# Kernel optimization log

Hardware: AMD Instinct MI355X
Metric: run time of the kernel (lower is better)

Reference implementation:

```python
import jax, jax.numpy as jnp
import numpy as np
from jax import lax

DIM = 192
HEADS = 6
WIDTH = 256
HEIGHT = 128
BATCH = 2


def _conv1x1(x, w):
    # x: [b,c,h,w], w: [o,c] (1x1 conv, no bias)
    return jnp.einsum('bchw,oc->bohw', x, w)


def setup_inputs() -> dict:
    key = jax.random.key(0)
    ks = jax.random.split(key, 7)
    c = DIM
    std = c ** -0.5
    x = jax.random.normal(ks[0], (BATCH, c, HEIGHT, WIDTH), dtype=jnp.float32)
    rpb_table = 0.02 * jax.random.normal(ks[1], (2 * WIDTH - 1, HEADS), dtype=jnp.float32)
    w_qkv = std * jax.random.normal(ks[2], (3 * c, c), dtype=jnp.float32)
    w_depth = (1.0 / 3.0) * jax.random.normal(ks[3], (3 * c, 1, 3, 3), dtype=jnp.float32)
    w_pre = std * jax.random.normal(ks[4], (c, c), dtype=jnp.float32)
    w_out = std * jax.random.normal(ks[5], (c, c), dtype=jnp.float32)
    w_gate = std * jax.random.normal(ks[6], (c, c), dtype=jnp.float32)
    return {"x": x, "rpb_table": rpb_table, "w_qkv": w_qkv, "w_depth": w_depth,
            "w_pre": w_pre, "w_out": w_out, "w_gate": w_gate, "num_heads": HEADS}


def reference(x, rpb_table, w_qkv, w_depth, w_pre, w_out, w_gate, num_heads):
    b, c, h, w = x.shape
    hd = c // num_heads
    scale = hd ** -0.5

    x_gate = jax.nn.silu(_conv1x1(x, w_gate))

    t = _conv1x1(x, w_qkv)  # [b, 3c, h, w]
    qkv = lax.conv_general_dilated(
        t, w_depth, window_strides=(1, 1), padding='SAME',
        feature_group_count=3 * c,
        dimension_numbers=('NCHW', 'OIHW', 'NCHW'))
    q, k, v = jnp.split(qkv, 3, axis=1)

    def _rows(z):
        # 'b (head c) h w -> b h head w c'
        return z.reshape(b, num_heads, hd, h, w).transpose(0, 3, 1, 4, 2)

    q = _rows(q) * scale
    k = _rows(k)
    v = _rows(v)

    attn = jnp.einsum('bhnic,bhnjc->bhnij', q, k)  # [b, h, heads, w, w]

    # relative position bias: index[i, j] = i - j + (w - 1)
    idx = jnp.arange(w)[:, None] - jnp.arange(w)[None, :] + (w - 1)
    bias = rpb_table[idx].transpose(2, 0, 1)  # [heads, w, w]
    attn = jax.nn.softmax(attn + bias[None, None], axis=-1)

    out = jnp.einsum('bhnij,bhnjc->bhnic', attn, v)
    # 'b h head w c -> b (head c) h w'
    out = out.transpose(0, 2, 4, 1, 3).reshape(b, c, h, w)

    out = _conv1x1(out, w_pre) * x_gate
    return _conv1x1(out, w_out)
```

## Files before the change

kernel.cpp:

```cpp
#include <hip/hip_runtime.h>
#include <hip/hip_bf16.h>
#include <math.h>

#define BATCH 2
#define C 192
#define H 128
#define W 256
#define HEADS 6
#define HD 32
#define HW (H * W)
#define C3 (3 * C)
#define NPX (BATCH * HW)

typedef unsigned short ushort_t;
using bf16x8 = __attribute__((ext_vector_type(8))) short;
using f32x4  = __attribute__((ext_vector_type(4))) float;

static __device__ __forceinline__ float bfbits2f(ushort_t u) {
    return __uint_as_float(((unsigned)u) << 16);
}
static __device__ __forceinline__ ushort_t f2bfbits(float f) {
    __hip_bfloat16 h = __float2bfloat16(f);
    return *reinterpret_cast<ushort_t*>(&h);
}

__global__ __launch_bounds__(256) void prep_w_kernel(
    const float* __restrict__ wq, const float* __restrict__ wg,
    const float* __restrict__ wp, const float* __restrict__ wo,
    ushort_t* __restrict__ dst)
{
    const int i = blockIdx.x * 256 + threadIdx.x;
    const float* src; int off, base;
    if (i < 27648)      { src = wq; off = i;         base = 0; }
    else if (i < 36864) { src = wg; off = i - 27648; base = 110592; }
    else if (i < 46080) { src = wp; off = i - 36864; base = 147456; }
    else                { src = wo; off = i - 46080; base = 184320; }
    float4 v = ((const float4*)src)[off];
    if (i < 9216) {
        const float sc = 0.25503488f;
        v.x *= sc; v.y *= sc; v.z *= sc; v.w *= sc;
    }
    ushort4 o;
    o.x = f2bfbits(v.x); o.y = f2bfbits(v.y);
    o.z = f2bfbits(v.z); o.w = f2bfbits(v.w);
    *(ushort4*)(dst + base + off * 4) = o;
}

__global__ __launch_bounds__(256) void transpose_x_kernel(
    const float* __restrict__ x, ushort_t* __restrict__ xt)
{
    __shared__ uint Xs[64 * 97];
    const int p0 = blockIdx.x * 64;
    const int b  = p0 >> 15, hw0 = p0 & (HW - 1);
    const int t  = threadIdx.x;

    {
        const int px = t & 63, g = t >> 6;
        const float* xb = x + (size_t)b * C * HW + hw0 + px;
#pragma unroll
        for (int i = 0; i < 24; ++i) {
            const int cp = g + i * 4;
            const float v0 = xb[(size_t)(2 * cp) * HW];
            const float v1 = xb[(size_t)(2 * cp + 1) * HW];
            Xs[px * 97 + cp] = (uint)f2bfbits(v0) | ((uint)f2bfbits(v1) << 16);
        }
    }
    __syncthreads();
    {
        const int px = t >> 2, grp = t & 3;
        uint* dst = (uint*)(xt + (size_t)(p0 + px) * C) + grp * 24;
        const uint* s = &Xs[px * 97 + grp * 24];
#pragma unroll
        for (int i = 0; i < 6; ++i) {
            uint4 u;
            u.x = s[i * 4 + 0]; u.y = s[i * 4 + 1];
            u.z = s[i * 4 + 2]; u.w = s[i * 4 + 3];
            *(uint4*)(dst + i * 4) = u;
        }
    }
}

template <int MODE, int OUTKIND, int MT>
__global__ __launch_bounds__(256, 2) void conv_mfma_kernel(
    const ushort_t* __restrict__ in_t, const ushort_t* __restrict__ w_bf,
    void* __restrict__ outp, ushort_t* __restrict__ gate, int ostride)
{
    const int lin = blockIdx.x;
    const int xcd = lin & 7;
    const int jj  = lin >> 3;
    const int pin = jj / MT;
    const int m   = jj - pin * MT;
    const int m0  = m * 64;
    const int p0  = (xcd * 32 + pin) * 256;

    const int t  = threadIdx.x;
    const int wv = t >> 6, lane = t & 63, quad = lane >> 4, l16 = lane & 15;

    __shared__ ushort_t smem[18432];
    ushort_t* As = smem;

    const ushort_t* bp = in_t + (size_t)(p0 + wv * 64 + l16) * C + quad * 8;
    bf16x8 bF[6][4];
#pragma unroll
    for (int ks = 0; ks < 6; ++ks)
#pragma unroll
        for (int ct = 0; ct < 4; ++ct)
            bF[ks][ct] = *(const bf16x8*)(bp + (size_t)(ct * 16) * C + ks * 32);

    {
        const int row = t >> 2, cg = (t & 3) * 48;
        const ushort_t* src = w_bf + (size_t)(m0 + row) * C + cg;
        ushort_t* dst = &As[row * 200 + cg];
#pragma unroll
        for (int i = 0; i < 6; ++i)
            *(bf16x8*)(dst + i * 8) = *(const bf16x8*)(src + i * 8);
    }
    __syncthreads();

    f32x4 acc[4][4];
#pragma unroll
    for (int rt = 0; rt < 4; ++rt)
#pragma unroll
        for (int ct = 0; ct < 4; ++ct) acc[rt][ct] = f32x4{0.f, 0.f, 0.f, 0.f};

#pragma unroll
    for (int ks = 0; ks < 6; ++ks) {
        bf16x8 aF[4];
#pragma unroll
        for (int rt = 0; rt < 4; ++rt)
            aF[rt] = *(const bf16x8*)&As[(rt * 16 + l16) * 200 + quad * 8 + ks * 32];
#pragma unroll
        for (int rt = 0; rt < 4; ++rt)
#pragma unroll
            for (int ct = 0; ct < 4; ++ct)
                acc[rt][ct] = __builtin_amdgcn_mfma_f32_16x16x32_bf16(
                    aF[rt], bF[ks][ct], acc[rt][ct], 0, 0, 0);
    }

    const bool isg = (MODE == 3) && (m >= 9);
    if (MODE == 1 || isg) {
#pragma unroll
        for (int rt = 0; rt < 4; ++rt)
#pragma unroll
            for (int ct = 0; ct < 4; ++ct) {
                f32x4 v = acc[rt][ct];
#pragma unroll
                for (int r = 0; r < 4; ++r)
                    v[r] = v[r] / (1.f + __expf(-v[r]));
                acc[rt][ct] = v;
            }
    }

    if constexpr (OUTKIND == 0) {
        __syncthreads();
        ushort_t* Ls = smem;
#pragma unroll
        for (int rt = 0; rt < 4; ++rt)
#pragma unroll
            for (int ct = 0; ct < 4; ++ct) {
                const f32x4 v = acc[rt][ct];
                ushort4 o;
                o.x = f2bfbits(v[0]); o.y = f2bfbits(v[1]);
                o.z = f2bfbits(v[2]); o.w = f2bfbits(v[3]);
                *(ushort4*)&Ls[(wv * 64 + ct * 16 + l16) * 72 +
                               rt * 16 + quad * 4] = o;
            }
        __syncthreads();

        ushort_t* ob; int osr, chb;
        if constexpr (MODE == 3) {
            ob  = isg ? gate : (ushort_t*)outp;
            osr = isg ? C : C3;
            chb = isg ? m0 - C3 : m0;
        } else {
            ob = (ushort_t*)outp; osr = ostride; chb = m0;
        }
        const int pxl = t >> 3, c8 = (t & 7) * 8;
#pragma unroll
        for (int r = 0; r < 8; ++r) {
            const int px = r * 32 + pxl;
            const bf16x8 v = *(const bf16x8*)&Ls[px * 72 + c8];
            *(bf16x8*)(ob + (size_t)(p0 + px) * osr + chb + c8) = v;
        }
    } else {
        const int bb = p0 >> 15;
        const int hwb = (p0 & (HW - 1)) + wv * 64;
        float* ob = (float*)outp + ((size_t)bb * C + m0) * HW + hwb;
#pragma unroll
        for (int rt = 0; rt < 4; ++rt)
#pragma unroll
            for (int ct = 0; ct < 4; ++ct) {
                const f32x4 v = acc[rt][ct];
#pragma unroll
                for (int r = 0; r < 4; ++r)
                    ob[(size_t)(rt * 16 + quad * 4 + r) * HW + ct * 16 + l16] = v[r];
            }
    }
}

__global__ __launch_bounds__(256) void dwconv3x3_px_kernel(
    const ushort_t* __restrict__ tin, const float* __restrict__ wd,
    ushort_t* __restrict__ out)
{
    __shared__ float wloc[576];
    __shared__ ushort_t Ld[128 * 72];
    const int bx = blockIdx.x;
    const int px_blk = (bx & 7) * 64 + (63 - (bx >> 3));
    const int cb  = blockIdx.y;
    const int tid = threadIdx.x;
    if (tid < 144)
        *(float4*)&wloc[tid * 4] = *(const float4*)(wd + cb * 576 + tid * 4);
    __syncthreads();

    const int chloc = (tid & 7) * 8;
    const int pxl0 = (tid >> 3) * 4;
    const int px = px_blk * 128 + pxl0;
    const int x0 = px & (W - 1);
    const int y  = (px >> 8) & (H - 1);

    const ushort_t* tb = tin + (size_t)px * C3 + cb * 64 + chloc;

    float acc[4][8];
#pragma unroll
    for (int i = 0; i < 4; ++i)
#pragma unroll
        for (int k = 0; k < 8; ++k) acc[i][k] = 0.f;

#pragma unroll
    for (int dy = -1; dy <= 1; ++dy) {
        const int yy = y + dy;
        if (yy < 0 || yy >= H) continue;
        const ushort_t* rp = tb + (ptrdiff_t)dy * W * C3;

        float f[6][8];
#pragma unroll
        for (int d = 0; d < 6; ++d) {
            const int xx = x0 + d - 1;
            if (xx < 0 || xx >= W) {
#pragma unroll
                for (int k = 0; k < 8; ++k) f[d][k] = 0.f;
            } else {
                const bf16x8 v = *(const bf16x8*)(rp + (ptrdiff_t)(d - 1) * C3);
#pragma unroll
                for (int k = 0; k < 8; ++k) f[d][k] = bfbits2f((ushort_t)v[k]);
            }
        }
#pragma unroll
        for (int k = 0; k < 8; ++k) {
            const float* wk = &wloc[(chloc + k) * 9 + (dy + 1) * 3];
            const float w0 = wk[0], w1 = wk[1], w2 = wk[2];
#pragma unroll
            for (int i = 0; i < 4; ++i)
                acc[i][k] += f[i][k] * w0 + f[i + 1][k] * w1 + f[i + 2][k] * w2;
        }
    }

#pragma unroll
    for (int i = 0; i < 4; ++i) {
        bf16x8 o;
#pragma unroll
        for (int k = 0; k < 8; ++k) o[k] = (short)f2bfbits(acc[i][k]);
        *(bf16x8*)&Ld[(pxl0 + i) * 72 + chloc] = o;
    }
    __syncthreads();

    const int pxl = tid >> 3, c8 = (tid & 7) * 8;
#pragma unroll
    for (int r = 0; r < 4; ++r) {
        const int p = r * 32 + pxl;
        const bf16x8 v = *(const bf16x8*)&Ld[p * 72 + c8];
        *(bf16x8*)(out + (size_t)(px_blk * 128 + p) * C3 + cb * 64 + c8) = v;
    }
}

__global__ __launch_bounds__(256, 4) void attention_mfma_kernel(
    const ushort_t* __restrict__ qkv, const float* __restrict__ rpb,
    ushort_t* __restrict__ att)
{
    const int lin  = blockIdx.x;
    const int xcd  = lin & 7;
    const int j    = lin >> 3;
    const int b    = xcd >> 2;
    const int y    = (xcd & 3) * 32 + (j & 31);
    const int head = j >> 5;
    const int t    = threadIdx.x;
    const int wv   = t >> 6;
    const int lane = t & 63;
    const int quad = lane >> 4;
    const int l16  = lane & 15;

    __shared__ __align__(16) char smem[39424];
    ushort_t* Vt = (ushort_t*)smem;
    ushort_t* Pb = (ushort_t*)(smem + 16896);
    ushort_t* rb = (ushort_t*)(smem + 37376);
    float*    Ol = (float*)smem;

    const size_t rowbase = ((size_t)b * HW + (size_t)y * W) * C3;
    const ushort_t* qbase = qkv + rowbase + head * HD + quad * 8;
    const ushort_t* kbase = qbase + C;

    {
        const ushort_t* rowp = qkv + rowbase + (size_t)t * C3 + head * HD;
        bf16x8 vfr[4];
#pragma unroll
        for (int g = 0; g < 4; ++g)
            vfr[g] = *(const bf16x8*)(rowp + 2 * C + g * 8);
#pragma unroll
        for (int g = 0; g < 4; ++g)
#pragma unroll
            for (int k = 0; k < 8; ++k)
                Vt[(g * 8 + k) * 264 + t] = (ushort_t)vfr[g][k];
    }
    {
        const float LOG2E = 1.4426950408889634f;
#pragma unroll
        for (int s2 = 0; s2 < 2; ++s2)
#pragma unroll
            for (int pp = 0; pp < 2; ++pp) {
                const int k = pp * 256 + t;
                const int src = k + s2;
                rb[s2 * 512 + k] =
                    f2bfbits(src <= 510 ? rpb[src * HEADS + head] * LOG2E : 0.f);
            }
    }

    bf16x8 aQ[4];
#pragma unroll
    for (int rt = 0; rt < 4; ++rt)
        aQ[rt] = *(const bf16x8*)(qbase + (size_t)(wv * 64 + rt * 16 + l16) * C3);
    bf16x8 bK = *(const bf16x8*)(kbase + (size_t)l16 * C3);

    __syncthreads();

    ushort_t* PbW = Pb + wv * 2560;
    float lsum[4] = {0.f, 0.f, 0.f, 0.f};
    f32x4 o_acc[4][2];
#pragma unroll
    for (int rt = 0; rt < 4; ++rt)
#pragma unroll
        for (int ct = 0; ct < 2; ++ct)
            o_acc[rt][ct] = f32x4{0.f, 0.f, 0.f, 0.f};

    const int ibase = wv * 64 + l16 + 255 - quad * 4;

    for (int c2 = 0; c2 < 8; ++c2) {
#pragma unroll
        for (int half = 0; half < 2; ++half) {
            const int n  = c2 * 2 + half;
            const int nn = (n < 15) ? n + 1 : 15;
            const bf16x8 bKn =
                *(const bf16x8*)(kbase + (size_t)(nn * 16 + l16) * C3);
#pragma unroll
            for (int rt = 0; rt < 4; ++rt) {
                const int a  = ibase + rt * 16 - n * 16 - 3;
                const int s2 = a & 1;
                const uint* tp = (const uint*)(rb + s2 * 512 + (a - s2));
                const uint u0 = tp[0], u1 = tp[1];
                f32x4 s;
                s[0] = __uint_as_float(u1 & 0xffff0000u);
                s[1] = __uint_as_float(u1 << 16);
                s[2] = __uint_as_float(u0 & 0xffff0000u);
                s[3] = __uint_as_float(u0 << 16);
                s = __builtin_amdgcn_mfma_f32_16x16x32_bf16(bK, aQ[rt], s, 0, 0, 0);
                const float p0 = __builtin_amdgcn_exp2f(s[0]);
                const float p1 = __builtin_amdgcn_exp2f(s[1]);
                const float p2 = __builtin_amdgcn_exp2f(s[2]);
                const float p3 = __builtin_amdgcn_exp2f(s[3]);
                lsum[rt] += (p0 + p1) + (p2 + p3);
                uint2 dd;
                dd.x = (uint)f2bfbits(p0) | ((uint)f2bfbits(p1) << 16);
                dd.y = (uint)f2bfbits(p2) | ((uint)f2bfbits(p3) << 16);
                *(uint2*)&PbW[(rt * 16 + l16) * 40 + half * 16 + quad * 4] = dd;
            }
            bK = bKn;
        }
#pragma unroll
        for (int rt = 0; rt < 4; ++rt) {
            const bf16x8 aP = *(const bf16x8*)&PbW[(rt * 16 + l16) * 40 + quad * 8];
#pragma unroll
            for (int ct = 0; ct < 2; ++ct) {
                const bf16x8 bV = *(const bf16x8*)
                    &Vt[(ct * 16 + l16) * 264 + c2 * 32 + quad * 8];
                o_acc[rt][ct] = __builtin_amdgcn_mfma_f32_16x16x32_bf16(
                    aP, bV, o_acc[rt][ct], 0, 0, 0);
            }
        }
    }

    float linv[4];
#pragma unroll
    for (int rt = 0; rt < 4; ++rt) {
        float v = lsum[rt];
        v += __shfl_xor(v, 16);
        v += __shfl_xor(v, 32);
        linv[rt] = 1.f / v;
    }

    __syncthreads();
#pragma unroll
    for (int rt = 0; rt < 4; ++rt) {
        const int i = wv * 64 + rt * 16 + quad * 4;
        float sc[4];
#pragma unroll
        for (int reg = 0; reg < 4; ++reg)
            sc[reg] = __shfl(linv[rt], quad * 4 + reg);
#pragma unroll
        for (int ct = 0; ct < 2; ++ct) {
            const int c = ct * 16 + l16;
#pragma unroll
            for (int reg = 0; reg < 4; ++reg)
                Ol[c * 257 + i + reg] = o_acc[rt][ct][reg] * sc[reg];
        }
    }
    __syncthreads();

    const size_t orow = (size_t)b * HW + (size_t)y * W;
    const int pxl = t >> 2, part = t & 3;
#pragma unroll
    for (int r = 0; r < 4; ++r) {
        const int px = r * 64 + pxl;
        bf16x8 o;
#pragma unroll
        for (int k = 0; k < 8; ++k)
            o[k] = (short)f2bfbits(Ol[(part * 8 + k) * 257 + px]);
        *(bf16x8*)(att + (orow + px) * C + head * HD + part * 8) = o;
    }
}

__global__ __launch_bounds__(256, 3) void conv2_fused_kernel(
    const ushort_t* __restrict__ att_t, const ushort_t* __restrict__ gatep,
    const ushort_t* __restrict__ wpre, const ushort_t* __restrict__ wout,
    float* __restrict__ outp)
{
    const int lin = blockIdx.x;
    const int xcd = lin & 7;
    const int pin = lin >> 3;
    const int p0  = (xcd * 64 + pin) * 128;

    const int t  = threadIdx.x;
    const int wv = t >> 6, lane = t & 63, quad = lane >> 4, l16 = lane & 15;

    __shared__ ushort_t Zs[4][32 * 200];
    ushort_t* Zw = Zs[wv];
    const int pxw = p0 + wv * 32;

#pragma unroll
    for (int ms = 0; ms < 3; ++ms) {
        f32x4 acc[4][2];
#pragma unroll
        for (int rt = 0; rt < 4; ++rt)
#pragma unroll
            for (int ct = 0; ct < 2; ++ct) acc[rt][ct] = f32x4{0.f,0.f,0.f,0.f};

        const ushort_t* ap = wpre + (size_t)(ms * 64 + l16) * C + quad * 8;
        const ushort_t* bp = att_t + (size_t)(pxw + l16) * C + quad * 8;
#pragma unroll
        for (int ks = 0; ks < 6; ++ks) {
            bf16x8 aF[4];
#pragma unroll
            for (int rt = 0; rt < 4; ++rt)
                aF[rt] = *(const bf16x8*)(ap + (size_t)(rt * 16) * C + ks * 32);
            const bf16x8 b0 = *(const bf16x8*)(bp + ks * 32);
            const bf16x8 b1 = *(const bf16x8*)(bp + (size_t)16 * C + ks * 32);
#pragma unroll
            for (int rt = 0; rt < 4; ++rt) {
                acc[rt][0] = __builtin_amdgcn_mfma_f32_16x16x32_bf16(
                    aF[rt], b0, acc[rt][0], 0, 0, 0);
                acc[rt][1] = __builtin_amdgcn_mfma_f32_16x16x32_bf16(
                    aF[rt], b1, acc[rt][1], 0, 0, 0);
            }
        }
#pragma unroll
        for (int rt = 0; rt < 4; ++rt)
#pragma unroll
            for (int ct = 0; ct < 2; ++ct) {
                const int px = pxw + ct * 16 + l16;
                const int ch = ms * 64 + rt * 16 + quad * 4;
                const ushort4 g = *(const ushort4*)(gatep + (size_t)px * C + ch);
                f32x4 v = acc[rt][ct];
                v[0] *= bfbits2f(g.x); v[1] *= bfbits2f(g.y);
                v[2] *= bfbits2f(g.z); v[3] *= bfbits2f(g.w);
                ushort4 o;
                o.x = f2bfbits(v[0]); o.y = f2bfbits(v[1]);
                o.z = f2bfbits(v[2]); o.w = f2bfbits(v[3]);
                *(ushort4*)&Zw[(ct * 16 + l16) * 200 + ch] = o;
            }
    }

    const int bb  = p0 >> 15;
    const int hwb = (p0 & (HW - 1)) + wv * 32;
#pragma unroll
    for (int ms = 0; ms < 3; ++ms) {
        f32x4 acc[4][2];
#pragma unroll
        for (int rt = 0; rt < 4; ++rt)
#pragma unroll
            for (int ct = 0; ct < 2; ++ct) acc[rt][ct] = f32x4{0.f,0.f,0.f,0.f};

        const ushort_t* ap = wout + (size_t)(ms * 64 + l16) * C + quad * 8;
#pragma unroll
        for (int ks = 0; ks < 6; ++ks) {
            bf16x8 aF[4];
#pragma unroll
            for (int rt = 0; rt < 4; ++rt)
                aF[rt] = *(const bf16x8*)(ap + (size_t)(rt * 16) * C + ks * 32);
            const bf16x8 b0 = *(const bf16x8*)&Zw[l16 * 200 + quad * 8 + ks * 32];
            const bf16x8 b1 = *(const bf16x8*)&Zw[(16 + l16) * 200 + quad * 8 + ks * 32];
#pragma unroll
            for (int rt = 0; rt < 4; ++rt) {
                acc[rt][0] = __builtin_amdgcn_mfma_f32_16x16x32_bf16(
                    aF[rt], b0, acc[rt][0], 0, 0, 0);
                acc[rt][1] = __builtin_amdgcn_mfma_f32_16x16x32_bf16(
                    aF[rt], b1, acc[rt][1], 0, 0, 0);
            }
        }
        float* ob = outp + ((size_t)bb * C + ms * 64) * HW + hwb;
#pragma unroll
        for (int rt = 0; rt < 4; ++rt)
#pragma unroll
            for (int ct = 0; ct < 2; ++ct) {
                const f32x4 v = acc[rt][ct];
#pragma unroll
                for (int r = 0; r < 4; ++r)
                    __builtin_nontemporal_store(v[r],
                        &ob[(size_t)(rt * 16 + quad * 4 + r) * HW + ct * 16 + l16]);
            }
    }
}

extern "C" void kernel_launch(void* const* d_in, const int* in_sizes, int n_in,
                              void* d_out, int out_size, void* d_ws, size_t ws_size,
                              hipStream_t stream)
{
    const float* x       = (const float*)d_in[0];
    const float* rpb     = (const float*)d_in[1];
    const float* w_qkv   = (const float*)d_in[2];
    const float* w_depth = (const float*)d_in[3];
    const float* w_pre   = (const float*)d_in[4];
    const float* w_out   = (const float*)d_in[5];
    const float* w_gate  = (const float*)d_in[6];
    float* out = (float*)d_out;

    char* wsb = (char*)d_ws;
    ushort_t* wbf      = (ushort_t*)wsb;
    ushort_t* w_pre_b  = wbf + 147456;
    ushort_t* w_out_b  = wbf + 184320;
    ushort_t* gate_t   = (ushort_t*)(wsb + 524288u);
    ushort_t* buf_t    = (ushort_t*)(wsb + 25690112u);
    ushort_t* att_t    = (ushort_t*)(wsb + 25690112u);
    ushort_t* buf_qkv  = (ushort_t*)(wsb + 101187584u);
    ushort_t* x_t      = (ushort_t*)(wsb + 101187584u);

    dim3 blk(256);

    prep_w_kernel<<<dim3(216), blk, 0, stream>>>(w_qkv, w_gate, w_pre, w_out, wbf);
    transpose_x_kernel<<<dim3(NPX / 64), blk, 0, stream>>>(x, x_t);
    conv_mfma_kernel<3, 0, 12><<<dim3(3072), blk, 0, stream>>>(
        x_t, wbf, buf_t, gate_t, C3);
    dwconv3x3_px_kernel<<<dim3(NPX / 128, 9), blk, 0, stream>>>(
        buf_t, w_depth, buf_qkv);
    attention_mfma_kernel<<<dim3(H * HEADS * BATCH), blk, 0, stream>>>(
        buf_qkv, rpb, att_t);
    conv2_fused_kernel<<<dim3(NPX / 128), blk, 0, stream>>>(
        att_t, gate_t, w_pre_b, w_out_b, out);
}
```

Baseline: 285.6 us.

## Batch global loads ahead of use with asm barriers across all kernels

Adds an empty inline-asm KEEP macro that pins loaded values in registers, so each kernel issues all of its global loads before any consumer arithmetic. This applies to the x transpose, the weight staging in the GEMM, the depthwise conv taps (now loaded unconditionally, with a zero fill at the borders), the V staging, the K prefetch and the output GEMMs. The output GEMMs also load their A fragments in two halves of three k-steps and pad the Z LDS stride from 200 to 204. The intent is more memory-level parallelism and fewer serialized load-use stalls, at the cost of higher register pressure and possibly lower occupancy.

```diff
diff --git a/kernel.cpp b/kernel.cpp
--- a/kernel.cpp
+++ b/kernel.cpp
@@ -15,6 +15,8 @@
 typedef unsigned short ushort_t;
 using bf16x8 = __attribute__((ext_vector_type(8))) short;
 using f32x4  = __attribute__((ext_vector_type(4))) float;
+
+#define KEEP(x) asm volatile("" : "+v"(x))
 
 static __device__ __forceinline__ float bfbits2f(ushort_t u) {
     return __uint_as_float(((unsigned)u) << 16);
@@ -57,12 +59,19 @@
     {
         const int px = t & 63, g = t >> 6;
         const float* xb = x + (size_t)b * C * HW + hw0 + px;
+        float va[24], vb[24];
 #pragma unroll
         for (int i = 0; i < 24; ++i) {
             const int cp = g + i * 4;
-            const float v0 = xb[(size_t)(2 * cp) * HW];
-            const float v1 = xb[(size_t)(2 * cp + 1) * HW];
-            Xs[px * 97 + cp] = (uint)f2bfbits(v0) | ((uint)f2bfbits(v1) << 16);
+            va[i] = xb[(size_t)(2 * cp) * HW];
+            vb[i] = xb[(size_t)(2 * cp + 1) * HW];
+        }
+#pragma unroll
+        for (int i = 0; i < 24; ++i) { KEEP(va[i]); KEEP(vb[i]); }
+#pragma unroll
+        for (int i = 0; i < 24; ++i) {
+            const int cp = g + i * 4;
+            Xs[px * 97 + cp] = (uint)f2bfbits(va[i]) | ((uint)f2bfbits(vb[i]) << 16);
         }
     }
     __syncthreads();
@@ -106,14 +115,24 @@
 #pragma unroll
         for (int ct = 0; ct < 4; ++ct)
             bF[ks][ct] = *(const bf16x8*)(bp + (size_t)(ct * 16) * C + ks * 32);
+#pragma unroll
+    for (int ks = 0; ks < 6; ++ks)
+#pragma unroll
+        for (int ct = 0; ct < 4; ++ct) KEEP(bF[ks][ct]);
 
     {
         const int row = t >> 2, cg = (t & 3) * 48;
         const ushort_t* src = w_bf + (size_t)(m0 + row) * C + cg;
+        bf16x8 wreg[6];
+#pragma unroll
+        for (int i = 0; i < 6; ++i)
+            wreg[i] = *(const bf16x8*)(src + i * 8);
+#pragma unroll
+        for (int i = 0; i < 6; ++i) KEEP(wreg[i]);
         ushort_t* dst = &As[row * 200 + cg];
 #pragma unroll
         for (int i = 0; i < 6; ++i)
-            *(bf16x8*)(dst + i * 8) = *(const bf16x8*)(src + i * 8);
+            *(bf16x8*)(dst + i * 8) = wreg[i];
     }
     __syncthreads();
 
@@ -220,34 +239,41 @@
 
     const ushort_t* tb = tin + (size_t)px * C3 + cb * 64 + chloc;
 
-    float acc[4][8];
-#pragma unroll
-    for (int i = 0; i < 4; ++i)
-#pragma unroll
-        for (int k = 0; k < 8; ++k) acc[i][k] = 0.f;
-
-#pragma unroll
-    for (int dy = -1; dy <= 1; ++dy) {
-        const int yy = y + dy;
-        if (yy < 0 || yy >= H) continue;
-        const ushort_t* rp = tb + (ptrdiff_t)dy * W * C3;
-
-        float f[6][8];
+    bf16x8 raw[3][6];
+#pragma unroll
+    for (int dy = 0; dy < 3; ++dy) {
+        const int yy = y + dy - 1;
+        const ushort_t* rp = tb + (ptrdiff_t)(dy - 1) * W * C3;
 #pragma unroll
         for (int d = 0; d < 6; ++d) {
             const int xx = x0 + d - 1;
-            if (xx < 0 || xx >= W) {
-#pragma unroll
-                for (int k = 0; k < 8; ++k) f[d][k] = 0.f;
-            } else {
-                const bf16x8 v = *(const bf16x8*)(rp + (ptrdiff_t)(d - 1) * C3);
-#pragma unroll
-                for (int k = 0; k < 8; ++k) f[d][k] = bfbits2f((ushort_t)v[k]);
-            }
-        }
+            bf16x8 v = bf16x8{0, 0, 0, 0, 0, 0, 0, 0};
+            if (yy >= 0 && yy < H && xx >= 0 && xx < W)
+                v = *(const bf16x8*)(rp + (ptrdiff_t)(d - 1) * C3);
+            raw[dy][d] = v;
+        }
+    }
+#pragma unroll
+    for (int dy = 0; dy < 3; ++dy)
+#pragma unroll
+        for (int d = 0; d < 6; ++d) KEEP(raw[dy][d]);
+
+    float acc[4][8];
+#pragma unroll
+    for (int i = 0; i < 4; ++i)
+#pragma unroll
+        for (int k = 0; k < 8; ++k) acc[i][k] = 0.f;
+
+#pragma unroll
+    for (int dy = 0; dy < 3; ++dy) {
+        float f[6][8];
+#pragma unroll
+        for (int d = 0; d < 6; ++d)
+#pragma unroll
+            for (int k = 0; k < 8; ++k) f[d][k] = bfbits2f((ushort_t)raw[dy][d][k]);
 #pragma unroll
         for (int k = 0; k < 8; ++k) {
-            const float* wk = &wloc[(chloc + k) * 9 + (dy + 1) * 3];
+            const float* wk = &wloc[(chloc + k) * 9 + dy * 3];
             const float w0 = wk[0], w1 = wk[1], w2 = wk[2];
 #pragma unroll
             for (int i = 0; i < 4; ++i)
@@ -306,6 +332,8 @@
         for (int g = 0; g < 4; ++g)
             vfr[g] = *(const bf16x8*)(rowp + 2 * C + g * 8);
 #pragma unroll
+        for (int g = 0; g < 4; ++g) KEEP(vfr[g]);
+#pragma unroll
         for (int g = 0; g < 4; ++g)
 #pragma unroll
             for (int k = 0; k < 8; ++k)
@@ -348,8 +376,8 @@
         for (int half = 0; half < 2; ++half) {
             const int n  = c2 * 2 + half;
             const int nn = (n < 15) ? n + 1 : 15;
-            const bf16x8 bKn =
-                *(const bf16x8*)(kbase + (size_t)(nn * 16 + l16) * C3);
+            bf16x8 bKn = *(const bf16x8*)(kbase + (size_t)(nn * 16 + l16) * C3);
+            KEEP(bKn);
 #pragma unroll
             for (int rt = 0; rt < 4; ++rt) {
                 const int a  = ibase + rt * 16 - n * 16 - 3;
@@ -440,7 +468,7 @@
     const int t  = threadIdx.x;
     const int wv = t >> 6, lane = t & 63, quad = lane >> 4, l16 = lane & 15;
 
-    __shared__ ushort_t Zs[4][32 * 200];
+    __shared__ ushort_t Zs[4][32 * 204];
     ushort_t* Zw = Zs[wv];
     const int pxw = p0 + wv * 32;
 
@@ -454,36 +482,65 @@
 
         const ushort_t* ap = wpre + (size_t)(ms * 64 + l16) * C + quad * 8;
         const ushort_t* bp = att_t + (size_t)(pxw + l16) * C + quad * 8;
+
+        bf16x8 bB[6][2];
 #pragma unroll
         for (int ks = 0; ks < 6; ++ks) {
-            bf16x8 aF[4];
-#pragma unroll
-            for (int rt = 0; rt < 4; ++rt)
-                aF[rt] = *(const bf16x8*)(ap + (size_t)(rt * 16) * C + ks * 32);
-            const bf16x8 b0 = *(const bf16x8*)(bp + ks * 32);
-            const bf16x8 b1 = *(const bf16x8*)(bp + (size_t)16 * C + ks * 32);
-#pragma unroll
-            for (int rt = 0; rt < 4; ++rt) {
-                acc[rt][0] = __builtin_amdgcn_mfma_f32_16x16x32_bf16(
-                    aF[rt], b0, acc[rt][0], 0, 0, 0);
-                acc[rt][1] = __builtin_amdgcn_mfma_f32_16x16x32_bf16(
-                    aF[rt], b1, acc[rt][1], 0, 0, 0);
-            }
-        }
+            bB[ks][0] = *(const bf16x8*)(bp + ks * 32);
+            bB[ks][1] = *(const bf16x8*)(bp + (size_t)16 * C + ks * 32);
+        }
+#pragma unroll
+        for (int ks = 0; ks < 6; ++ks) { KEEP(bB[ks][0]); KEEP(bB[ks][1]); }
+
+#pragma unroll
+        for (int h = 0; h < 2; ++h) {
+            bf16x8 aF[3][4];
+#pragma unroll
+            for (int k2 = 0; k2 < 3; ++k2)
+#pragma unroll
+                for (int rt = 0; rt < 4; ++rt)
+                    aF[k2][rt] = *(const bf16x8*)(ap + (size_t)(rt * 16) * C +
+                                                  (h * 3 + k2) * 32);
+#pragma unroll
+            for (int k2 = 0; k2 < 3; ++k2)
+#pragma unroll
+                for (int rt = 0; rt < 4; ++rt) KEEP(aF[k2][rt]);
+#pragma unroll
+            for (int k2 = 0; k2 < 3; ++k2)
+#pragma unroll
+                for (int rt = 0; rt < 4; ++rt) {
+                    acc[rt][0] = __builtin_amdgcn_mfma_f32_16x16x32_bf16(
+                        aF[k2][rt], bB[h * 3 + k2][0], acc[rt][0], 0, 0, 0);
+                    acc[rt][1] = __builtin_amdgcn_mfma_f32_16x16x32_bf16(
+                        aF[k2][rt], bB[h * 3 + k2][1], acc[rt][1], 0, 0, 0);
+                }
+        }
+
+        ushort4 g[4][2];
 #pragma unroll
         for (int rt = 0; rt < 4; ++rt)
 #pragma unroll
             for (int ct = 0; ct < 2; ++ct) {
                 const int px = pxw + ct * 16 + l16;
                 const int ch = ms * 64 + rt * 16 + quad * 4;
-                const ushort4 g = *(const ushort4*)(gatep + (size_t)px * C + ch);
+                g[rt][ct] = *(const ushort4*)(gatep + (size_t)px * C + ch);
+            }
+#pragma unroll
+        for (int rt = 0; rt < 4; ++rt)
+#pragma unroll
+            for (int ct = 0; ct < 2; ++ct) KEEP(g[rt][ct]);
+#pragma unroll
+        for (int rt = 0; rt < 4; ++rt)
+#pragma unroll
+            for (int ct = 0; ct < 2; ++ct) {
+                const int ch = ms * 64 + rt * 16 + quad * 4;
                 f32x4 v = acc[rt][ct];
-                v[0] *= bfbits2f(g.x); v[1] *= bfbits2f(g.y);
-                v[2] *= bfbits2f(g.z); v[3] *= bfbits2f(g.w);
+                v[0] *= bfbits2f(g[rt][ct].x); v[1] *= bfbits2f(g[rt][ct].y);
+                v[2] *= bfbits2f(g[rt][ct].z); v[3] *= bfbits2f(g[rt][ct].w);
                 ushort4 o;
                 o.x = f2bfbits(v[0]); o.y = f2bfbits(v[1]);
                 o.z = f2bfbits(v[2]); o.w = f2bfbits(v[3]);
-                *(ushort4*)&Zw[(ct * 16 + l16) * 200 + ch] = o;
+                *(ushort4*)&Zw[(ct * 16 + l16) * 204 + ch] = o;
             }
     }
 
@@ -499,19 +556,30 @@
 
         const ushort_t* ap = wout + (size_t)(ms * 64 + l16) * C + quad * 8;
 #pragma unroll
-        for (int ks = 0; ks < 6; ++ks) {
-            bf16x8 aF[4];
-#pragma unroll
-            for (int rt = 0; rt < 4; ++rt)
-                aF[rt] = *(const bf16x8*)(ap + (size_t)(rt * 16) * C + ks * 32);
-            const bf16x8 b0 = *(const bf16x8*)&Zw[l16 * 200 + quad * 8 + ks * 32];
-            const bf16x8 b1 = *(const bf16x8*)&Zw[(16 + l16) * 200 + quad * 8 + ks * 32];
-#pragma unroll
-            for (int rt = 0; rt < 4; ++rt) {
-                acc[rt][0] = __builtin_amdgcn_mfma_f32_16x16x32_bf16(
-                    aF[rt], b0, acc[rt][0], 0, 0, 0);
-                acc[rt][1] = __builtin_amdgcn_mfma_f32_16x16x32_bf16(
-                    aF[rt], b1, acc[rt][1], 0, 0, 0);
+        for (int h = 0; h < 2; ++h) {
+            bf16x8 aF[3][4];
+#pragma unroll
+            for (int k2 = 0; k2 < 3; ++k2)
+#pragma unroll
+                for (int rt = 0; rt < 4; ++rt)
+                    aF[k2][rt] = *(const bf16x8*)(ap + (size_t)(rt * 16) * C +
+                                                  (h * 3 + k2) * 32);
+#pragma unroll
+            for (int k2 = 0; k2 < 3; ++k2)
+#pragma unroll
+                for (int rt = 0; rt < 4; ++rt) KEEP(aF[k2][rt]);
+#pragma unroll
+            for (int k2 = 0; k2 < 3; ++k2) {
+                const int ks = h * 3 + k2;
+                const bf16x8 b0 = *(const bf16x8*)&Zw[l16 * 204 + quad * 8 + ks * 32];
+                const bf16x8 b1 = *(const bf16x8*)&Zw[(16 + l16) * 204 + quad * 8 + ks * 32];
+#pragma unroll
+                for (int rt = 0; rt < 4; ++rt) {
+                    acc[rt][0] = __builtin_amdgcn_mfma_f32_16x16x32_bf16(
+                        aF[k2][rt], b0, acc[rt][0], 0, 0, 0);
+                    acc[rt][1] = __builtin_amdgcn_mfma_f32_16x16x32_bf16(
+                        aF[k2][rt], b1, acc[rt][1], 0, 0, 0);
+                }
             }
         }
         float* ob = outp + ((size_t)bb * C + ms * 64) * HW + hwb;
```

Result: slower. 293.2 us (+2.7%).

## Restructure first 1x1 conv to keep pixel tile resident and loop over all outputs

Applied to the files above, without the earlier changes.

The first pointwise conv (qkv plus gate) moves from a grid of 3072 blocks, each handling a 64-channel by 256-pixel tile, to 512 blocks that each keep a 128-pixel activation tile in registers and loop over all 12 output-channel groups. Weights are now read straight from global memory into registers instead of being staged through LDS. This avoids re-reading the input pixels once per output group, at the cost of fewer, longer blocks and more weight traffic from L2. The fused second conv kernel also hoists its activation fragments out of the output-group loop, batches weight loads in halves, and pads its LDS row stride from 200 to 204 to reduce bank conflicts.

```diff
diff --git a/kernel.cpp b/kernel.cpp
--- a/kernel.cpp
+++ b/kernel.cpp
@@ -80,121 +80,94 @@
     }
 }
 
-template <int MODE, int OUTKIND, int MT>
-__global__ __launch_bounds__(256, 2) void conv_mfma_kernel(
+__global__ __launch_bounds__(256, 2) void conv1_all_kernel(
     const ushort_t* __restrict__ in_t, const ushort_t* __restrict__ w_bf,
-    void* __restrict__ outp, ushort_t* __restrict__ gate, int ostride)
+    ushort_t* __restrict__ outp, ushort_t* __restrict__ gate)
 {
     const int lin = blockIdx.x;
     const int xcd = lin & 7;
-    const int jj  = lin >> 3;
-    const int pin = jj / MT;
-    const int m   = jj - pin * MT;
-    const int m0  = m * 64;
-    const int p0  = (xcd * 32 + pin) * 256;
+    const int pin = lin >> 3;
+    const int p0  = (xcd * 64 + pin) * 128;
 
     const int t  = threadIdx.x;
     const int wv = t >> 6, lane = t & 63, quad = lane >> 4, l16 = lane & 15;
-
-    __shared__ ushort_t smem[18432];
-    ushort_t* As = smem;
-
-    const ushort_t* bp = in_t + (size_t)(p0 + wv * 64 + l16) * C + quad * 8;
-    bf16x8 bF[6][4];
-#pragma unroll
-    for (int ks = 0; ks < 6; ++ks)
-#pragma unroll
-        for (int ct = 0; ct < 4; ++ct)
-            bF[ks][ct] = *(const bf16x8*)(bp + (size_t)(ct * 16) * C + ks * 32);
-
-    {
-        const int row = t >> 2, cg = (t & 3) * 48;
-        const ushort_t* src = w_bf + (size_t)(m0 + row) * C + cg;
-        ushort_t* dst = &As[row * 200 + cg];
-#pragma unroll
-        for (int i = 0; i < 6; ++i)
-            *(bf16x8*)(dst + i * 8) = *(const bf16x8*)(src + i * 8);
-    }
-    __syncthreads();
-
-    f32x4 acc[4][4];
-#pragma unroll
-    for (int rt = 0; rt < 4; ++rt)
-#pragma unroll
-        for (int ct = 0; ct < 4; ++ct) acc[rt][ct] = f32x4{0.f, 0.f, 0.f, 0.f};
-
+    const int pxw = p0 + wv * 32;
+
+    __shared__ ushort_t Ls[128 * 72];
+
+    const ushort_t* bp = in_t + (size_t)(pxw + l16) * C + quad * 8;
+    bf16x8 bB[6][2];
 #pragma unroll
     for (int ks = 0; ks < 6; ++ks) {
-        bf16x8 aF[4];
+        bB[ks][0] = *(const bf16x8*)(bp + ks * 32);
+        bB[ks][1] = *(const bf16x8*)(bp + (size_t)16 * C + ks * 32);
+    }
+
+#pragma unroll
+    for (int m = 0; m < 12; ++m) {
+        const int m0 = m * 64;
+        const ushort_t* ap = w_bf + (size_t)(m0 + l16) * C + quad * 8;
+
+        bf16x8 aF[6][4];
+#pragma unroll
+        for (int ks = 0; ks < 6; ++ks)
+#pragma unroll
+            for (int rt = 0; rt < 4; ++rt)
+                aF[ks][rt] = *(const bf16x8*)(ap + (size_t)(rt * 16) * C + ks * 32);
+
+        f32x4 acc[4][2];
 #pragma unroll
         for (int rt = 0; rt < 4; ++rt)
-            aF[rt] = *(const bf16x8*)&As[(rt * 16 + l16) * 200 + quad * 8 + ks * 32];
+#pragma unroll
+            for (int ct = 0; ct < 2; ++ct) acc[rt][ct] = f32x4{0.f,0.f,0.f,0.f};
+
+#pragma unroll
+        for (int ks = 0; ks < 6; ++ks)
+#pragma unroll
+            for (int rt = 0; rt < 4; ++rt) {
+                acc[rt][0] = __builtin_amdgcn_mfma_f32_16x16x32_bf16(
+                    aF[ks][rt], bB[ks][0], acc[rt][0], 0, 0, 0);
+                acc[rt][1] = __builtin_amdgcn_mfma_f32_16x16x32_bf16(
+                    aF[ks][rt], bB[ks][1], acc[rt][1], 0, 0, 0);
+            }
+
+        if (m >= 9) {
+#pragma unroll
+            for (int rt = 0; rt < 4; ++rt)
+#pragma unroll
+                for (int ct = 0; ct < 2; ++ct) {
+                    f32x4 v = acc[rt][ct];
+#pragma unroll
+                    for (int r = 0; r < 4; ++r)
+                        v[r] = v[r] / (1.f + __expf(-v[r]));
+                    acc[rt][ct] = v;
+                }
+        }
+
+        __syncthreads();
 #pragma unroll
         for (int rt = 0; rt < 4; ++rt)
 #pragma unroll
-            for (int ct = 0; ct < 4; ++ct)
-                acc[rt][ct] = __builtin_amdgcn_mfma_f32_16x16x32_bf16(
-                    aF[rt], bF[ks][ct], acc[rt][ct], 0, 0, 0);
-    }
-
-    const bool isg = (MODE == 3) && (m >= 9);
-    if (MODE == 1 || isg) {
-#pragma unroll
-        for (int rt = 0; rt < 4; ++rt)
-#pragma unroll
-            for (int ct = 0; ct < 4; ++ct) {
-                f32x4 v = acc[rt][ct];
-#pragma unroll
-                for (int r = 0; r < 4; ++r)
-                    v[r] = v[r] / (1.f + __expf(-v[r]));
-                acc[rt][ct] = v;
-            }
-    }
-
-    if constexpr (OUTKIND == 0) {
-        __syncthreads();
-        ushort_t* Ls = smem;
-#pragma unroll
-        for (int rt = 0; rt < 4; ++rt)
-#pragma unroll
-            for (int ct = 0; ct < 4; ++ct) {
+            for (int ct = 0; ct < 2; ++ct) {
                 const f32x4 v = acc[rt][ct];
                 ushort4 o;
                 o.x = f2bfbits(v[0]); o.y = f2bfbits(v[1]);
                 o.z = f2bfbits(v[2]); o.w = f2bfbits(v[3]);
-                *(ushort4*)&Ls[(wv * 64 + ct * 16 + l16) * 72 +
+                *(ushort4*)&Ls[(wv * 32 + ct * 16 + l16) * 72 +
                                rt * 16 + quad * 4] = o;
             }
         __syncthreads();
 
         ushort_t* ob; int osr, chb;
-        if constexpr (MODE == 3) {
-            ob  = isg ? gate : (ushort_t*)outp;
-            osr = isg ? C : C3;
-            chb = isg ? m0 - C3 : m0;
-        } else {
-            ob = (ushort_t*)outp; osr = ostride; chb = m0;
-        }
+        if (m < 9) { ob = outp; osr = C3; chb = m0; }
+        else       { ob = gate; osr = C;  chb = m0 - C3; }
         const int pxl = t >> 3, c8 = (t & 7) * 8;
 #pragma unroll
-        for (int r = 0; r < 8; ++r) {
+        for (int r = 0; r < 4; ++r) {
             const int px = r * 32 + pxl;
             const bf16x8 v = *(const bf16x8*)&Ls[px * 72 + c8];
             *(bf16x8*)(ob + (size_t)(p0 + px) * osr + chb + c8) = v;
         }
-    } else {
-        const int bb = p0 >> 15;
-        const int hwb = (p0 & (HW - 1)) + wv * 64;
-        float* ob = (float*)outp + ((size_t)bb * C + m0) * HW + hwb;
-#pragma unroll
-        for (int rt = 0; rt < 4; ++rt)
-#pragma unroll
-            for (int ct = 0; ct < 4; ++ct) {
-                const f32x4 v = acc[rt][ct];
-#pragma unroll
-                for (int r = 0; r < 4; ++r)
-                    ob[(size_t)(rt * 16 + quad * 4 + r) * HW + ct * 16 + l16] = v[r];
-            }
     }
 }
 
@@ -440,10 +413,18 @@
     const int t  = threadIdx.x;
     const int wv = t >> 6, lane = t & 63, quad = lane >> 4, l16 = lane & 15;
 
-    __shared__ ushort_t Zs[4][32 * 200];
+    __shared__ ushort_t Zs[4][32 * 204];
     ushort_t* Zw = Zs[wv];
     const int pxw = p0 + wv * 32;
 
+    const ushort_t* bp = att_t + (size_t)(pxw + l16) * C + quad * 8;
+    bf16x8 bB[6][2];
+#pragma unroll
+    for (int ks = 0; ks < 6; ++ks) {
+        bB[ks][0] = *(const bf16x8*)(bp + ks * 32);
+        bB[ks][1] = *(const bf16x8*)(bp + (size_t)16 * C + ks * 32);
+    }
+
 #pragma unroll
     for (int ms = 0; ms < 3; ++ms) {
         f32x4 acc[4][2];
@@ -453,23 +434,26 @@
             for (int ct = 0; ct < 2; ++ct) acc[rt][ct] = f32x4{0.f,0.f,0.f,0.f};
 
         const ushort_t* ap = wpre + (size_t)(ms * 64 + l16) * C + quad * 8;
-        const ushort_t* bp = att_t + (size_t)(pxw + l16) * C + quad * 8;
-#pragma unroll
-        for (int ks = 0; ks < 6; ++ks) {
-            bf16x8 aF[4];
-#pragma unroll
-            for (int rt = 0; rt < 4; ++rt)
-                aF[rt] = *(const bf16x8*)(ap + (size_t)(rt * 16) * C + ks * 32);
-            const bf16x8 b0 = *(const bf16x8*)(bp + ks * 32);
-            const bf16x8 b1 = *(const bf16x8*)(bp + (size_t)16 * C + ks * 32);
-#pragma unroll
-            for (int rt = 0; rt < 4; ++rt) {
-                acc[rt][0] = __builtin_amdgcn_mfma_f32_16x16x32_bf16(
-                    aF[rt], b0, acc[rt][0], 0, 0, 0);
-                acc[rt][1] = __builtin_amdgcn_mfma_f32_16x16x32_bf16(
-                    aF[rt], b1, acc[rt][1], 0, 0, 0);
-            }
-        }
+#pragma unroll
+        for (int h = 0; h < 2; ++h) {
+            bf16x8 aF[3][4];
+#pragma unroll
+            for (int k2 = 0; k2 < 3; ++k2)
+#pragma unroll
+                for (int rt = 0; rt < 4; ++rt)
+                    aF[k2][rt] = *(const bf16x8*)(ap + (size_t)(rt * 16) * C +
+                                                  (h * 3 + k2) * 32);
+#pragma unroll
+            for (int k2 = 0; k2 < 3; ++k2)
+#pragma unroll
+                for (int rt = 0; rt < 4; ++rt) {
+                    acc[rt][0] = __builtin_amdgcn_mfma_f32_16x16x32_bf16(
+                        aF[k2][rt], bB[h * 3 + k2][0], acc[rt][0], 0, 0, 0);
+                    acc[rt][1] = __builtin_amdgcn_mfma_f32_16x16x32_bf16(
+                        aF[k2][rt], bB[h * 3 + k2][1], acc[rt][1], 0, 0, 0);
+                }
+        }
+
 #pragma unroll
         for (int rt = 0; rt < 4; ++rt)
 #pragma unroll
@@ -483,7 +467,7 @@
                 ushort4 o;
                 o.x = f2bfbits(v[0]); o.y = f2bfbits(v[1]);
                 o.z = f2bfbits(v[2]); o.w = f2bfbits(v[3]);
-                *(ushort4*)&Zw[(ct * 16 + l16) * 200 + ch] = o;
+                *(ushort4*)&Zw[(ct * 16 + l16) * 204 + ch] = o;
             }
     }
 
@@ -499,19 +483,26 @@
 
         const ushort_t* ap = wout + (size_t)(ms * 64 + l16) * C + quad * 8;
 #pragma unroll
-        for (int ks = 0; ks < 6; ++ks) {
-            bf16x8 aF[4];
-#pragma unroll
-            for (int rt = 0; rt < 4; ++rt)
-                aF[rt] = *(const bf16x8*)(ap + (size_t)(rt * 16) * C + ks * 32);
-            const bf16x8 b0 = *(const bf16x8*)&Zw[l16 * 200 + quad * 8 + ks * 32];
-            const bf16x8 b1 = *(const bf16x8*)&Zw[(16 + l16) * 200 + quad * 8 + ks * 32];
-#pragma unroll
-            for (int rt = 0; rt < 4; ++rt) {
-                acc[rt][0] = __builtin_amdgcn_mfma_f32_16x16x32_bf16(
-                    aF[rt], b0, acc[rt][0], 0, 0, 0);
-                acc[rt][1] = __builtin_amdgcn_mfma_f32_16x16x32_bf16(
-                    aF[rt], b1, acc[rt][1], 0, 0, 0);
+        for (int h = 0; h < 2; ++h) {
+            bf16x8 aF[3][4];
+#pragma unroll
+            for (int k2 = 0; k2 < 3; ++k2)
+#pragma unroll
+                for (int rt = 0; rt < 4; ++rt)
+                    aF[k2][rt] = *(const bf16x8*)(ap + (size_t)(rt * 16) * C +
+                                                  (h * 3 + k2) * 32);
+#pragma unroll
+            for (int k2 = 0; k2 < 3; ++k2) {
+                const int ks = h * 3 + k2;
+                const bf16x8 b0 = *(const bf16x8*)&Zw[l16 * 204 + quad * 8 + ks * 32];
+                const bf16x8 b1 = *(const bf16x8*)&Zw[(16 + l16) * 204 + quad * 8 + ks * 32];
+#pragma unroll
+                for (int rt = 0; rt < 4; ++rt) {
+                    acc[rt][0] = __builtin_amdgcn_mfma_f32_16x16x32_bf16(
+                        aF[k2][rt], b0, acc[rt][0], 0, 0, 0);
+                    acc[rt][1] = __builtin_amdgcn_mfma_f32_16x16x32_bf16(
+                        aF[k2][rt], b1, acc[rt][1], 0, 0, 0);
+                }
             }
         }
         float* ob = outp + ((size_t)bb * C + ms * 64) * HW + hwb;
@@ -555,8 +546,8 @@
 
     prep_w_kernel<<<dim3(216), blk, 0, stream>>>(w_qkv, w_gate, w_pre, w_out, wbf);
     transpose_x_kernel<<<dim3(NPX / 64), blk, 0, stream>>>(x, x_t);
-    conv_mfma_kernel<3, 0, 12><<<dim3(3072), blk, 0, stream>>>(
-        x_t, wbf, buf_t, gate_t, C3);
+    conv1_all_kernel<<<dim3(NPX / 128), blk, 0, stream>>>(
+        x_t, wbf, buf_t, gate_t);
     dwconv3x3_px_kernel<<<dim3(NPX / 128, 9), blk, 0, stream>>>(
         buf_t, w_depth, buf_qkv);
     attention_mfma_kernel<<<dim3(H * HEADS * BATCH), blk, 0, stream>>>(
```

After: 325.5 us. 1.14x slower.

## Fuse depthwise 3x3 conv into attention kernel and restructure conv2 operand loads

Applied to the files above, without the earlier changes.

Removes the standalone depthwise conv kernel and computes the 3x3 depthwise conv for q, k and v of one row/head inside the attention block. The results are staged in shared memory (Q, K, transposed V), which drops a full write and re-read of the 3C-channel qkv tensor through global memory. Block-to-work mapping changes so heads of the same row sit next to each other, which improves L2 reuse of the three neighbouring input rows. The conv2 kernel now preloads its activation B-fragments once into registers, batches A-weight loads, and pads the LDS stride to 204. The trade-offs are larger shared memory use (occupancy set to 2 blocks per SM) and the 3x3 halo rows being recomputed or reloaded per block.

```diff
diff --git a/kernel.cpp b/kernel.cpp
--- a/kernel.cpp
+++ b/kernel.cpp
@@ -198,118 +198,35 @@
     }
 }
 
-__global__ __launch_bounds__(256) void dwconv3x3_px_kernel(
+__global__ __launch_bounds__(256, 2) void attention_dw_kernel(
     const ushort_t* __restrict__ tin, const float* __restrict__ wd,
-    ushort_t* __restrict__ out)
-{
-    __shared__ float wloc[576];
-    __shared__ ushort_t Ld[128 * 72];
-    const int bx = blockIdx.x;
-    const int px_blk = (bx & 7) * 64 + (63 - (bx >> 3));
-    const int cb  = blockIdx.y;
-    const int tid = threadIdx.x;
-    if (tid < 144)
-        *(float4*)&wloc[tid * 4] = *(const float4*)(wd + cb * 576 + tid * 4);
-    __syncthreads();
-
-    const int chloc = (tid & 7) * 8;
-    const int pxl0 = (tid >> 3) * 4;
-    const int px = px_blk * 128 + pxl0;
-    const int x0 = px & (W - 1);
-    const int y  = (px >> 8) & (H - 1);
-
-    const ushort_t* tb = tin + (size_t)px * C3 + cb * 64 + chloc;
-
-    float acc[4][8];
-#pragma unroll
-    for (int i = 0; i < 4; ++i)
-#pragma unroll
-        for (int k = 0; k < 8; ++k) acc[i][k] = 0.f;
-
-#pragma unroll
-    for (int dy = -1; dy <= 1; ++dy) {
-        const int yy = y + dy;
-        if (yy < 0 || yy >= H) continue;
-        const ushort_t* rp = tb + (ptrdiff_t)dy * W * C3;
-
-        float f[6][8];
-#pragma unroll
-        for (int d = 0; d < 6; ++d) {
-            const int xx = x0 + d - 1;
-            if (xx < 0 || xx >= W) {
-#pragma unroll
-                for (int k = 0; k < 8; ++k) f[d][k] = 0.f;
-            } else {
-                const bf16x8 v = *(const bf16x8*)(rp + (ptrdiff_t)(d - 1) * C3);
-#pragma unroll
-                for (int k = 0; k < 8; ++k) f[d][k] = bfbits2f((ushort_t)v[k]);
-            }
-        }
-#pragma unroll
-        for (int k = 0; k < 8; ++k) {
-            const float* wk = &wloc[(chloc + k) * 9 + (dy + 1) * 3];
-            const float w0 = wk[0], w1 = wk[1], w2 = wk[2];
-#pragma unroll
-            for (int i = 0; i < 4; ++i)
-                acc[i][k] += f[i][k] * w0 + f[i + 1][k] * w1 + f[i + 2][k] * w2;
-        }
-    }
-
-#pragma unroll
-    for (int i = 0; i < 4; ++i) {
-        bf16x8 o;
-#pragma unroll
-        for (int k = 0; k < 8; ++k) o[k] = (short)f2bfbits(acc[i][k]);
-        *(bf16x8*)&Ld[(pxl0 + i) * 72 + chloc] = o;
-    }
-    __syncthreads();
-
-    const int pxl = tid >> 3, c8 = (tid & 7) * 8;
-#pragma unroll
-    for (int r = 0; r < 4; ++r) {
-        const int p = r * 32 + pxl;
-        const bf16x8 v = *(const bf16x8*)&Ld[p * 72 + c8];
-        *(bf16x8*)(out + (size_t)(px_blk * 128 + p) * C3 + cb * 64 + c8) = v;
-    }
-}
-
-__global__ __launch_bounds__(256, 4) void attention_mfma_kernel(
-    const ushort_t* __restrict__ qkv, const float* __restrict__ rpb,
-    ushort_t* __restrict__ att)
+    const float* __restrict__ rpb, ushort_t* __restrict__ att)
 {
     const int lin  = blockIdx.x;
     const int xcd  = lin & 7;
     const int j    = lin >> 3;
     const int b    = xcd >> 2;
-    const int y    = (xcd & 3) * 32 + (j & 31);
-    const int head = j >> 5;
+    const int yl   = j / 6;
+    const int head = j - yl * 6;
+    const int y    = (xcd & 3) * 32 + yl;
     const int t    = threadIdx.x;
     const int wv   = t >> 6;
     const int lane = t & 63;
     const int quad = lane >> 4;
     const int l16  = lane & 15;
 
-    __shared__ __align__(16) char smem[39424];
-    ushort_t* Vt = (ushort_t*)smem;
-    ushort_t* Pb = (ushort_t*)(smem + 16896);
-    ushort_t* rb = (ushort_t*)(smem + 37376);
-    float*    Ol = (float*)smem;
-
-    const size_t rowbase = ((size_t)b * HW + (size_t)y * W) * C3;
-    const ushort_t* qbase = qkv + rowbase + head * HD + quad * 8;
-    const ushort_t* kbase = qbase + C;
-
-    {
-        const ushort_t* rowp = qkv + rowbase + (size_t)t * C3 + head * HD;
-        bf16x8 vfr[4];
-#pragma unroll
-        for (int g = 0; g < 4; ++g)
-            vfr[g] = *(const bf16x8*)(rowp + 2 * C + g * 8);
-#pragma unroll
-        for (int g = 0; g < 4; ++g)
-#pragma unroll
-            for (int k = 0; k < 8; ++k)
-                Vt[(g * 8 + k) * 264 + t] = (ushort_t)vfr[g][k];
+    __shared__ __align__(16) char smem[63360];
+    ushort_t* Ks  = (ushort_t*)smem;
+    ushort_t* Qs  = (ushort_t*)(smem + 20480);
+    ushort_t* Vt  = (ushort_t*)(smem + 40960);
+    ushort_t* rb  = (ushort_t*)(smem + 57856);
+    float*    wdl = (float*)(smem + 59904);
+    float*    Ol  = (float*)smem;
+
+    if (t < 216) {
+        const int s = t / 72, i = t - s * 72;
+        *(float4*)&wdl[s * 288 + i * 4] =
+            *(const float4*)(wd + (size_t)(s * 192 + head * HD) * 9 + i * 4);
     }
     {
         const float LOG2E = 1.4426950408889634f;
@@ -323,16 +240,59 @@
                     f2bfbits(src <= 510 ? rpb[src * HEADS + head] * LOG2E : 0.f);
             }
     }
+    __syncthreads();
+
+    {
+        const ushort_t* base = tin +
+            ((size_t)(b * HW + y * W) + t) * C3 + head * HD;
+#pragma unroll
+        for (int s = 0; s < 3; ++s) {
+#pragma unroll
+            for (int c8 = 0; c8 < 4; ++c8) {
+                float acc[8];
+#pragma unroll
+                for (int k = 0; k < 8; ++k) acc[k] = 0.f;
+#pragma unroll
+                for (int dy = -1; dy <= 1; ++dy) {
+                    const int yy = y + dy;
+                    if (yy < 0 || yy >= H) continue;
+                    const ushort_t* rp =
+                        base + (ptrdiff_t)dy * (W * C3) + s * C + c8 * 8;
+#pragma unroll
+                    for (int dx = -1; dx <= 1; ++dx) {
+                        const int xx = t + dx;
+                        if (xx < 0 || xx >= W) continue;
+                        const bf16x8 v = *(const bf16x8*)(rp + (ptrdiff_t)dx * C3);
+                        const float* wk =
+                            &wdl[(s * 32 + c8 * 8) * 9 + (dy + 1) * 3 + (dx + 1)];
+#pragma unroll
+                        for (int k = 0; k < 8; ++k)
+                            acc[k] += bfbits2f((ushort_t)v[k]) * wk[k * 9];
+                    }
+                }
+                if (s < 2) {
+                    bf16x8 o;
+#pragma unroll
+                    for (int k = 0; k < 8; ++k) o[k] = (short)f2bfbits(acc[k]);
+                    ushort_t* dst = (s == 0) ? Qs : Ks;
+                    *(bf16x8*)&dst[t * 40 + c8 * 8] = o;
+                } else {
+#pragma unroll
+                    for (int k = 0; k < 8; ++k)
+                        Vt[(c8 * 8 + k) * 264 + t] = f2bfbits(acc[k]);
+                }
+            }
+        }
+    }
+    __syncthreads();
 
     bf16x8 aQ[4];
 #pragma unroll
     for (int rt = 0; rt < 4; ++rt)
-        aQ[rt] = *(const bf16x8*)(qbase + (size_t)(wv * 64 + rt * 16 + l16) * C3);
-    bf16x8 bK = *(const bf16x8*)(kbase + (size_t)l16 * C3);
-
-    __syncthreads();
-
-    ushort_t* PbW = Pb + wv * 2560;
+        aQ[rt] = *(const bf16x8*)&Qs[(wv * 64 + rt * 16 + l16) * 40 + quad * 8];
+    __syncthreads();
+    ushort_t* PbW = Qs + wv * 2560;
+
     float lsum[4] = {0.f, 0.f, 0.f, 0.f};
     f32x4 o_acc[4][2];
 #pragma unroll
@@ -346,10 +306,8 @@
     for (int c2 = 0; c2 < 8; ++c2) {
 #pragma unroll
         for (int half = 0; half < 2; ++half) {
-            const int n  = c2 * 2 + half;
-            const int nn = (n < 15) ? n + 1 : 15;
-            const bf16x8 bKn =
-                *(const bf16x8*)(kbase + (size_t)(nn * 16 + l16) * C3);
+            const int n = c2 * 2 + half;
+            const bf16x8 bK = *(const bf16x8*)&Ks[(n * 16 + l16) * 40 + quad * 8];
 #pragma unroll
             for (int rt = 0; rt < 4; ++rt) {
                 const int a  = ibase + rt * 16 - n * 16 - 3;
@@ -372,7 +330,6 @@
                 dd.y = (uint)f2bfbits(p2) | ((uint)f2bfbits(p3) << 16);
                 *(uint2*)&PbW[(rt * 16 + l16) * 40 + half * 16 + quad * 4] = dd;
             }
-            bK = bKn;
         }
 #pragma unroll
         for (int rt = 0; rt < 4; ++rt) {
@@ -440,10 +397,18 @@
     const int t  = threadIdx.x;
     const int wv = t >> 6, lane = t & 63, quad = lane >> 4, l16 = lane & 15;
 
-    __shared__ ushort_t Zs[4][32 * 200];
+    __shared__ ushort_t Zs[4][32 * 204];
     ushort_t* Zw = Zs[wv];
     const int pxw = p0 + wv * 32;
 
+    const ushort_t* bp = att_t + (size_t)(pxw + l16) * C + quad * 8;
+    bf16x8 bB[6][2];
+#pragma unroll
+    for (int ks = 0; ks < 6; ++ks) {
+        bB[ks][0] = *(const bf16x8*)(bp + ks * 32);
+        bB[ks][1] = *(const bf16x8*)(bp + (size_t)16 * C + ks * 32);
+    }
+
 #pragma unroll
     for (int ms = 0; ms < 3; ++ms) {
         f32x4 acc[4][2];
@@ -453,23 +418,26 @@
             for (int ct = 0; ct < 2; ++ct) acc[rt][ct] = f32x4{0.f,0.f,0.f,0.f};
 
         const ushort_t* ap = wpre + (size_t)(ms * 64 + l16) * C + quad * 8;
-        const ushort_t* bp = att_t + (size_t)(pxw + l16) * C + quad * 8;
-#pragma unroll
-        for (int ks = 0; ks < 6; ++ks) {
-            bf16x8 aF[4];
-#pragma unroll
-            for (int rt = 0; rt < 4; ++rt)
-                aF[rt] = *(const bf16x8*)(ap + (size_t)(rt * 16) * C + ks * 32);
-            const bf16x8 b0 = *(const bf16x8*)(bp + ks * 32);
-            const bf16x8 b1 = *(const bf16x8*)(bp + (size_t)16 * C + ks * 32);
-#pragma unroll
-            for (int rt = 0; rt < 4; ++rt) {
-                acc[rt][0] = __builtin_amdgcn_mfma_f32_16x16x32_bf16(
-                    aF[rt], b0, acc[rt][0], 0, 0, 0);
-                acc[rt][1] = __builtin_amdgcn_mfma_f32_16x16x32_bf16(
-                    aF[rt], b1, acc[rt][1], 0, 0, 0);
-            }
-        }
+#pragma unroll
+        for (int h = 0; h < 2; ++h) {
+            bf16x8 aF[3][4];
+#pragma unroll
+            for (int k2 = 0; k2 < 3; ++k2)
+#pragma unroll
+                for (int rt = 0; rt < 4; ++rt)
+                    aF[k2][rt] = *(const bf16x8*)(ap + (size_t)(rt * 16) * C +
+                                                  (h * 3 + k2) * 32);
+#pragma unroll
+            for (int k2 = 0; k2 < 3; ++k2)
+#pragma unroll
+                for (int rt = 0; rt < 4; ++rt) {
+                    acc[rt][0] = __builtin_amdgcn_mfma_f32_16x16x32_bf16(
+                        aF[k2][rt], bB[h * 3 + k2][0], acc[rt][0], 0, 0, 0);
+                    acc[rt][1] = __builtin_amdgcn_mfma_f32_16x16x32_bf16(
+                        aF[k2][rt], bB[h * 3 + k2][1], acc[rt][1], 0, 0, 0);
+                }
+        }
+
 #pragma unroll
         for (int rt = 0; rt < 4; ++rt)
 #pragma unroll
@@ -483,7 +451,7 @@
                 ushort4 o;
                 o.x = f2bfbits(v[0]); o.y = f2bfbits(v[1]);
                 o.z = f2bfbits(v[2]); o.w = f2bfbits(v[3]);
-                *(ushort4*)&Zw[(ct * 16 + l16) * 200 + ch] = o;
+                *(ushort4*)&Zw[(ct * 16 + l16) * 204 + ch] = o;
             }
     }
 
@@ -499,19 +467,26 @@
 
         const ushort_t* ap = wout + (size_t)(ms * 64 + l16) * C + quad * 8;
 #pragma unroll
-        for (int ks = 0; ks < 6; ++ks) {
-            bf16x8 aF[4];
-#pragma unroll
-            for (int rt = 0; rt < 4; ++rt)
-                aF[rt] = *(const bf16x8*)(ap + (size_t)(rt * 16) * C + ks * 32);
-            const bf16x8 b0 = *(const bf16x8*)&Zw[l16 * 200 + quad * 8 + ks * 32];
-            const bf16x8 b1 = *(const bf16x8*)&Zw[(16 + l16) * 200 + quad * 8 + ks * 32];
-#pragma unroll
-            for (int rt = 0; rt < 4; ++rt) {
-                acc[rt][0] = __builtin_amdgcn_mfma_f32_16x16x32_bf16(
-                    aF[rt], b0, acc[rt][0], 0, 0, 0);
-                acc[rt][1] = __builtin_amdgcn_mfma_f32_16x16x32_bf16(
-                    aF[rt], b1, acc[rt][1], 0, 0, 0);
+        for (int h = 0; h < 2; ++h) {
+            bf16x8 aF[3][4];
+#pragma unroll
+            for (int k2 = 0; k2 < 3; ++k2)
+#pragma unroll
+                for (int rt = 0; rt < 4; ++rt)
+                    aF[k2][rt] = *(const bf16x8*)(ap + (size_t)(rt * 16) * C +
+                                                  (h * 3 + k2) * 32);
+#pragma unroll
+            for (int k2 = 0; k2 < 3; ++k2) {
+                const int ks = h * 3 + k2;
+                const bf16x8 b0 = *(const bf16x8*)&Zw[l16 * 204 + quad * 8 + ks * 32];
+                const bf16x8 b1 = *(const bf16x8*)&Zw[(16 + l16) * 204 + quad * 8 + ks * 32];
+#pragma unroll
+                for (int rt = 0; rt < 4; ++rt) {
+                    acc[rt][0] = __builtin_amdgcn_mfma_f32_16x16x32_bf16(
+                        aF[k2][rt], b0, acc[rt][0], 0, 0, 0);
+                    acc[rt][1] = __builtin_amdgcn_mfma_f32_16x16x32_bf16(
+                        aF[k2][rt], b1, acc[rt][1], 0, 0, 0);
+                }
             }
         }
         float* ob = outp + ((size_t)bb * C + ms * 64) * HW + hwb;
@@ -547,9 +522,8 @@
     ushort_t* w_out_b  = wbf + 184320;
     ushort_t* gate_t   = (ushort_t*)(wsb + 524288u);
     ushort_t* buf_t    = (ushort_t*)(wsb + 25690112u);
-    ushort_t* att_t    = (ushort_t*)(wsb + 25690112u);
-    ushort_t* buf_qkv  = (ushort_t*)(wsb + 101187584u);
     ushort_t* x_t      = (ushort_t*)(wsb + 101187584u);
+    ushort_t* att_t    = (ushort_t*)(wsb + 101187584u);
 
     dim3 blk(256);
 
@@ -557,10 +531,8 @@
     transpose_x_kernel<<<dim3(NPX / 64), blk, 0, stream>>>(x, x_t);
     conv_mfma_kernel<3, 0, 12><<<dim3(3072), blk, 0, stream>>>(
         x_t, wbf, buf_t, gate_t, C3);
-    dwconv3x3_px_kernel<<<dim3(NPX / 128, 9), blk, 0, stream>>>(
-        buf_t, w_depth, buf_qkv);
-    attention_mfma_kernel<<<dim3(H * HEADS * BATCH), blk, 0, stream>>>(
-        buf_qkv, rpb, att_t);
+    attention_dw_kernel<<<dim3(H * HEADS * BATCH), blk, 0, stream>>>(
+        buf_t, w_depth, rpb, att_t);
     conv2_fused_kernel<<<dim3(NPX / 128), blk, 0, stream>>>(
         att_t, gate_t, w_pre_b, w_out_b, out);
 }
```

After: 418.9 us. +46.7%, slower.
